# Performance work log

Hardware: AMD Instinct MI355X
Metric: run time of the kernel (lower is better)

## Reference

```python
import jax, jax.numpy as jnp
import numpy as np

EPS = 1e-5

def bn_relu(y, g, b):
    # BatchNorm1d in training mode: stats over (B, L) per channel, biased variance
    mu = jnp.mean(y, axis=(0, 2), keepdims=True)
    var = jnp.var(y, axis=(0, 2), keepdims=True)
    yn = (y - mu) * jax.lax.rsqrt(var + EPS)
    return jax.nn.relu(yn * g[None, :, None] + b[None, :, None])

def conv1x1_pad1(x, W):
    # Conv1d(k=1, padding=1, bias=False): pointwise matmul then zero-pad length by 1 each side
    y = jnp.einsum('bcl,oc->bol', x, W)
    return jnp.pad(y, ((0, 0), (0, 0), (1, 1)))

def conv1x1(x, W, b):
    return jnp.einsum('bcl,oc->bol', x, W) + b[None, :, None]

def conv3_pad1(x, W):
    # Conv1d(k=3, padding=1, bias=False); W: [O, C, 3]
    return jax.lax.conv_general_dilated(x, W, window_strides=(1,), padding=((1, 1),),
                                        dimension_numbers=('NCH', 'OIH', 'NCH'))

def pam(f, Wq, bq, Wk, bk, Wv, bv, gamma):
    q = conv1x1(f, Wq, bq)          # [B, C//8, L]
    k = conv1x1(f, Wk, bk)          # [B, C//8, L]
    v = conv1x1(f, Wv, bv)          # [B, C, L]
    energy = jnp.einsum('bql,bqm->blm', q, k)   # [B, L, L]
    attn = jax.nn.softmax(energy, axis=-1)
    out = jnp.einsum('bcm,blm->bcl', v, attn)
    return gamma * out + f

def cam(f, gamma):
    energy = jnp.einsum('bcl,bdl->bcd', f, f)    # [B, C, C]
    energy_new = jnp.max(energy, axis=-1, keepdims=True) - energy
    attn = jax.nn.softmax(energy_new, axis=-1)
    out = jnp.einsum('bcd,bdl->bcl', attn, f)
    return gamma * out + f

def setup_inputs() -> dict:
    key = jax.random.key(0)
    ks = jax.random.split(key, 24)
    B, C, L = 8, 256, 2046
    IC, OC = C // 4, 128  # inter_channels=64, out_channels
    s = 0.05
    d = {
        'x':   jax.random.normal(ks[0], (B, C, L), jnp.float32),
        'W5a': jax.random.normal(ks[1], (IC, C), jnp.float32) * s,
        'g5a': jnp.ones((IC,), jnp.float32), 'b5a': jnp.zeros((IC,), jnp.float32),
        'W5c': jax.random.normal(ks[2], (IC, C), jnp.float32) * s,
        'g5c': jnp.ones((IC,), jnp.float32), 'b5c': jnp.zeros((IC,), jnp.float32),
        'Wq':  jax.random.normal(ks[3], (IC // 8, IC), jnp.float32) * s,
        'bq':  jnp.zeros((IC // 8,), jnp.float32),
        'Wk':  jax.random.normal(ks[4], (IC // 8, IC), jnp.float32) * s,
        'bk':  jnp.zeros((IC // 8,), jnp.float32),
        'Wv':  jax.random.normal(ks[5], (IC, IC), jnp.float32) * s,
        'bv':  jnp.zeros((IC,), jnp.float32),
        'gamma_pam': jnp.full((1,), 0.1, jnp.float32),
        'gamma_cam': jnp.full((1,), 0.1, jnp.float32),
        'W51': jax.random.normal(ks[6], (IC, IC, 3), jnp.float32) * s,
        'g51': jnp.ones((IC,), jnp.float32), 'b51': jnp.zeros((IC,), jnp.float32),
        'W52': jax.random.normal(ks[7], (IC, IC, 3), jnp.float32) * s,
        'g52': jnp.ones((IC,), jnp.float32), 'b52': jnp.zeros((IC,), jnp.float32),
        'W6':  jax.random.normal(ks[8], (OC, IC), jnp.float32) * s,
        'b6':  jnp.zeros((OC,), jnp.float32),
        'W7':  jax.random.normal(ks[9], (OC, IC), jnp.float32) * s,
        'b7':  jnp.zeros((OC,), jnp.float32),
        'W8':  jax.random.normal(ks[10], (OC, IC), jnp.float32) * s,
        'b8':  jnp.zeros((OC,), jnp.float32),
    }
    return d

def reference(x, W5a, g5a, b5a, W5c, g5c, b5c, Wq, bq, Wk, bk, Wv, bv,
              gamma_pam, gamma_cam, W51, g51, b51, W52, g52, b52,
              W6, b6, W7, b7, W8, b8):
    # dropout (p=0.1) treated as identity (eval mode)
    feat1 = bn_relu(conv1x1_pad1(x, W5a), g5a, b5a)          # [B, IC, L+2]
    sa_feat = pam(feat1, Wq, bq, Wk, bk, Wv, bv, gamma_pam)
    sa_conv = bn_relu(conv3_pad1(sa_feat, W51), g51, b51)
    sa_output = conv1x1(sa_conv, W6, b6)                     # [B, OC, L+2]
    feat2 = bn_relu(conv1x1_pad1(x, W5c), g5c, b5c)
    sc_feat = cam(feat2, gamma_cam)
    sc_conv = bn_relu(conv3_pad1(sc_feat, W52), g52, b52)
    sc_output = conv1x1(sc_conv, W7, b7)
    feat_sum = sa_conv + sc_conv
    sasc = conv1x1(feat_sum, W8, b8)
    # pool == 'maxpool' selects AdaptiveAvgPool1d(1) in the original (note swap)
    sasc = jnp.mean(sasc, axis=-1)                            # [B, OC]
    return (sasc, sa_output, sc_output)
```

## Files before the change

### kernel.cpp

```cpp
#include <hip/hip_runtime.h>
#include <math.h>

#define B 8
#define C 256
#define L 2046
#define LP 2048
#define IC 64
#define OC 128
#define BN_EPS 1e-5f
#define INVN (1.f / 16384.f)

#define OFF_Y1T    0u
#define OFF_Y2C    524288u
#define OFF_SAFT   1048576u
#define OFF_SCFT   1572864u
#define OFF_Y51T   2097152u
#define OFF_Y52T   2621440u
#define OFF_VB     3145728u
#define OFF_QT     3670016u
#define OFF_KT     3735552u
#define OFF_LPART  3801088u
#define OFF_EPART  3866624u
#define OFF_ATTN   4390912u
#define OFF_STATS1 4423680u
#define OFF_STATS2 4424704u
#define OFF_W5BF   4425728u
#define OFF_W67    4442112u
#define OFF_WT     4450304u
#define OFF_WQKV   4462592u
#define OFF_BQKV   4465152u

typedef __attribute__((ext_vector_type(8))) short bshort8;
typedef __attribute__((ext_vector_type(4))) float f32x4;

__device__ __forceinline__ unsigned short f2bf(float f) {
    union { float f; unsigned int u; } v; v.f = f;
    return (unsigned short)((v.u + 0x8000u) >> 16);
}
__device__ __forceinline__ float bf2f(unsigned short u) {
    union { unsigned int i; float f; } v; v.i = ((unsigned int)u) << 16;
    return v.f;
}
__device__ __forceinline__ unsigned int pk2(float a, float b) {
    union { float f; unsigned int u; } va, vb; va.f = a; vb.f = b;
    return __builtin_amdgcn_perm(vb.u + 0x8000u, va.u + 0x8000u, 0x07060302u);
}

__device__ __forceinline__ void load_coef(const float* __restrict__ STATS,
        const float* __restrict__ g, const float* __restrict__ beta,
        int base, int cnt, float* cA, float* cB) {
    int t = threadIdx.x;
    if (t < cnt) {
        int ch = base + t;
        float s = STATS[ch * 2] + STATS[256 + ch * 2] + STATS[512 + ch * 2] + STATS[768 + ch * 2];
        float q = STATS[ch * 2 + 1] + STATS[256 + ch * 2 + 1] + STATS[512 + ch * 2 + 1] + STATS[768 + ch * 2 + 1];
        float mu = s * INVN;
        float var = q * INVN - mu * mu;
        float A = g[t] * rsqrtf(var + BN_EPS);
        cA[t] = A;
        cB[t] = beta[t] - mu * A;
    }
}

__global__ __launch_bounds__(256) void k_wprep(
        const float* __restrict__ W5a, const float* __restrict__ W5c,
        const float* __restrict__ W6, const float* __restrict__ W7,
        const float* __restrict__ W51, const float* __restrict__ W52,
        const float* __restrict__ Wq, const float* __restrict__ Wk,
        const float* __restrict__ Wv, const float* __restrict__ bq,
        const float* __restrict__ bk, const float* __restrict__ bv,
        const float* __restrict__ b8,
        unsigned short* __restrict__ W5BF, unsigned short* __restrict__ W67,
        unsigned short* __restrict__ WT, unsigned short* __restrict__ WQKV,
        float* __restrict__ BQKV, float* __restrict__ STATS1,
        float* __restrict__ STATS2, float* __restrict__ out_sasc) {
    int i = blockIdx.x * 256 + threadIdx.x;
    if (i < 32768) {
        int o = i >> 8, c = i & 255;
        W5BF[i] = f2bf(o < 64 ? W5a[o * 256 + c] : W5c[(o - 64) * 256 + c]);
    } else if (i < 49152) {
        int j = i - 32768; int g = j >> 13; int r = j & 8191;
        W67[j] = f2bf(g ? W7[r] : W6[r]);
    } else if (i < 73728) {
        int j = i - 49152;
        int c = j & 63, o = (j >> 6) & 63, wt = j >> 12; int w = wt / 3, t = wt % 3;
        const float* Ws = w ? W52 : W51;
        WT[j] = f2bf(Ws[(o * 64 + c) * 3 + t]);
    } else if (i < 78848) {
        int j = i - 73728; int o = j >> 6, c = j & 63;
        float v = o < 8 ? Wq[o * 64 + c] : (o < 16 ? Wk[(o - 8) * 64 + c] : Wv[(o - 16) * 64 + c]);
        WQKV[j] = f2bf(v);
    } else if (i < 78928) {
        int o = i - 78848;
        BQKV[o] = o < 8 ? bq[o] : (o < 16 ? bk[o - 8] : bv[o - 16]);
    } else if (i < 80976) {
        int j = i - 78928;
        if (j < 1024) STATS1[j] = 0.f; else STATS2[j - 1024] = 0.f;
    } else if (i < 82000) {
        int j = i - 80976;
        out_sasc[j] = b8[j & 127];
    }
}

__global__ __launch_bounds__(256) void k_conv1(const float* __restrict__ x,
        const unsigned short* __restrict__ W5BF,
        unsigned short* __restrict__ Y1T, unsigned short* __restrict__ Y2C,
        float* __restrict__ STATS1) {
    __shared__ unsigned short xt[64][264];
    __shared__ float lds_part[4][64];
    int lt = blockIdx.x, b = blockIdx.y;
    int l0 = lt * 64;
    int t = threadIdx.x;
    {
        int j = t & 63, cg = t >> 6;
        int ls = l0 - 1 + j;
        bool ok = (ls >= 0) && (ls < L);
        const float* xs = x + (size_t)(b * C + cg * 64) * L + ls;
        unsigned short* row = &xt[j][cg * 64];
#pragma unroll 8
        for (int cc = 0; cc < 64; ++cc) {
            float v = ok ? xs[(size_t)cc * L] : 0.f;
            row[cc] = f2bf(v);
        }
    }
    __syncthreads();
    int w = t >> 6, lane = t & 63, n = lane & 15, quad = lane >> 4;
    bshort8 wf[2][8];
#pragma unroll
    for (int oi = 0; oi < 2; ++oi)
#pragma unroll
        for (int kt = 0; kt < 8; ++kt)
            wf[oi][kt] = *(const bshort8*)(W5BF + (size_t)((w * 2 + oi) * 16 + n) * C + kt * 32 + quad * 8);
    f32x4 acc[2][4];
#pragma unroll
    for (int oi = 0; oi < 2; ++oi)
#pragma unroll
        for (int sub = 0; sub < 4; ++sub) acc[oi][sub] = (f32x4){0.f, 0.f, 0.f, 0.f};
#pragma unroll
    for (int sub = 0; sub < 4; ++sub) {
        int lloc = sub * 16 + n;
#pragma unroll
        for (int kt = 0; kt < 8; ++kt) {
            bshort8 xb = *(const bshort8*)(&xt[lloc][kt * 32 + quad * 8]);
            acc[0][sub] = __builtin_amdgcn_mfma_f32_16x16x32_bf16(wf[0][kt], xb, acc[0][sub], 0, 0, 0);
            acc[1][sub] = __builtin_amdgcn_mfma_f32_16x16x32_bf16(wf[1][kt], xb, acc[1][sub], 0, 0, 0);
        }
    }
    if (w < 2) {
#pragma unroll
        for (int sub = 0; sub < 4; ++sub) {
            int lp = l0 + sub * 16 + n;
#pragma unroll
            for (int oi = 0; oi < 2; ++oi) {
                int ot = w * 2 + oi;
                uint2 pv;
                pv.x = pk2(acc[oi][sub][0], acc[oi][sub][1]);
                pv.y = pk2(acc[oi][sub][2], acc[oi][sub][3]);
                *(uint2*)(Y1T + ((size_t)(b * LP + lp)) * IC + ot * 16 + quad * 4) = pv;
            }
        }
    } else {
#pragma unroll
        for (int oi = 0; oi < 2; ++oi) {
            int ot = (w - 2) * 2 + oi;
#pragma unroll
            for (int r = 0; r < 4; ++r) {
                int o = ot * 16 + quad * 4 + r;
                unsigned short* dst = Y2C + ((size_t)(b * IC + o)) * LP + l0;
#pragma unroll
                for (int sub = 0; sub < 4; ++sub)
                    dst[sub * 16 + n] = f2bf(acc[oi][sub][r]);
            }
        }
    }
#pragma unroll
    for (int oi = 0; oi < 2; ++oi)
#pragma unroll
        for (int r = 0; r < 4; ++r) {
            float s = 0.f, q = 0.f;
#pragma unroll
            for (int sub = 0; sub < 4; ++sub) {
                float v = acc[oi][sub][r];
                s += v; q += v * v;
            }
#pragma unroll
            for (int msk = 1; msk < 16; msk <<= 1) {
                s += __shfl_xor(s, msk, 64);
                q += __shfl_xor(q, msk, 64);
            }
            if (n == 0) {
                int ci = oi * 16 + quad * 4 + r;
                lds_part[w][ci * 2] = s;
                lds_part[w][ci * 2 + 1] = q;
            }
        }
    __syncthreads();
    {
        int ch = t >> 1, wsrc = ch >> 5;
        int idx = ((ch & 31) << 1) | (t & 1);
        atomicAdd(&STATS1[(blockIdx.x & 3) * 256 + t], lds_part[wsrc][idx]);
    }
}

__device__ void role_qkv(char* dynsm, int lt, int b,
        const unsigned short* __restrict__ Y1T, const float* __restrict__ STATS1,
        const float* __restrict__ g5a, const float* __restrict__ b5a,
        const unsigned short* __restrict__ WQKV, const float* __restrict__ BQKV,
        unsigned short* __restrict__ QT, unsigned short* __restrict__ KT,
        unsigned short* __restrict__ VB) {
    float* cA = (float*)dynsm;
    float* cB = cA + 64;
    load_coef(STATS1, g5a, b5a, 0, 64, cA, cB);
    __syncthreads();
    int t = threadIdx.x;
    int w = t >> 6, lane = t & 63, n = lane & 15, quad = lane >> 4;
    int lrow = lt * 64 + w * 16 + n;
    bshort8 fb[2];
#pragma unroll
    for (int kt = 0; kt < 2; ++kt) {
        bshort8 raw = *(const bshort8*)(Y1T + ((size_t)(b * LP + lrow)) * IC + kt * 32 + quad * 8);
        bshort8 f;
#pragma unroll
        for (int j = 0; j < 8; ++j) {
            int c = kt * 32 + quad * 8 + j;
            float v = fmaxf(fmaf(cA[c], bf2f((unsigned short)raw[j]), cB[c]), 0.f);
            ((unsigned short*)&f)[j] = f2bf(v);
        }
        fb[kt] = f;
    }
    f32x4 acc[5];
#pragma unroll
    for (int ot = 0; ot < 5; ++ot) {
        f32x4 a = {0.f, 0.f, 0.f, 0.f};
#pragma unroll
        for (int kt = 0; kt < 2; ++kt) {
            bshort8 wf = *(const bshort8*)(WQKV + (size_t)(ot * 16 + n) * IC + kt * 32 + quad * 8);
            a = __builtin_amdgcn_mfma_f32_16x16x32_bf16(wf, fb[kt], a, 0, 0, 0);
        }
        acc[ot] = a;
    }
#pragma unroll
    for (int ot = 0; ot < 5; ++ot)
#pragma unroll
        for (int r = 0; r < 4; ++r) {
            int o = ot * 16 + quad * 4 + r;
            unsigned short bv16 = f2bf(acc[ot][r] + BQKV[o]);
            if (ot == 0) {
                if (o < 8) QT[((size_t)(b * LP + lrow)) * 8 + o] = bv16;
                else KT[((size_t)(b * LP + lrow)) * 8 + (o - 8)] = bv16;
            } else {
                VB[((size_t)(b * IC + (o - 16))) * LP + lrow] = bv16;
            }
        }
}

__device__ void role_gram(char* dynsm, int blk, int b,
        const unsigned short* __restrict__ Y2C, const float* __restrict__ STATS1,
        const float* __restrict__ g5c, const float* __restrict__ b5c,
        float* __restrict__ EPART) {
    float* cA = (float*)dynsm;
    float* cB = cA + 64;
    load_coef(STATS1, g5c, b5c, 64, 64, cA, cB);
    __syncthreads();
    int t = threadIdx.x;
    int w = t >> 6, lane = t & 63, n = lane & 15, quad = lane >> 4;
    f32x4 acc[4][4];
#pragma unroll
    for (int ti = 0; ti < 4; ++ti)
#pragma unroll
        for (int tj = 0; tj < 4; ++tj) acc[ti][tj] = (f32x4){0.f, 0.f, 0.f, 0.f};
    for (int chunk = 0; chunk < 4; ++chunk) {
        int lb = (blk * 4 + w) * 128 + chunk * 32 + quad * 8;
        bshort8 frag[4];
#pragma unroll
        for (int g = 0; g < 4; ++g) {
            int c = g * 16 + n;
            bshort8 raw = *(const bshort8*)(Y2C + ((size_t)(b * IC + c)) * LP + lb);
            bshort8 f;
            float A = cA[c], Bc = cB[c];
#pragma unroll
            for (int j = 0; j < 8; ++j)
                ((unsigned short*)&f)[j] = f2bf(fmaxf(fmaf(A, bf2f((unsigned short)raw[j]), Bc), 0.f));
            frag[g] = f;
        }
#pragma unroll
        for (int ti = 0; ti < 4; ++ti)
#pragma unroll
            for (int tj = 0; tj < 4; ++tj)
                acc[ti][tj] = __builtin_amdgcn_mfma_f32_16x16x32_bf16(frag[ti], frag[tj], acc[ti][tj], 0, 0, 0);
    }
    float* ep = EPART + ((size_t)(b * 16 + blk * 4 + w)) * 4096;
#pragma unroll
    for (int ti = 0; ti < 4; ++ti)
#pragma unroll
        for (int tj = 0; tj < 4; ++tj)
#pragma unroll
            for (int r = 0; r < 4; ++r)
                ep[(ti * 16 + quad * 4 + r) * 64 + tj * 16 + n] = acc[ti][tj][r];
}

__global__ __launch_bounds__(256) void k_fuse1(
        const unsigned short* __restrict__ Y1T, const unsigned short* __restrict__ Y2C,
        const float* __restrict__ STATS1,
        const float* __restrict__ g5a, const float* __restrict__ b5a,
        const float* __restrict__ g5c, const float* __restrict__ b5c,
        const unsigned short* __restrict__ WQKV, const float* __restrict__ BQKV,
        unsigned short* __restrict__ QT, unsigned short* __restrict__ KT,
        unsigned short* __restrict__ VB, float* __restrict__ EPART) {
    extern __shared__ char dynsm[];
    int idx = blockIdx.x;
    if (idx < 256) role_qkv(dynsm, idx & 31, idx >> 5, Y1T, STATS1, g5a, b5a,
                            WQKV, BQKV, QT, KT, VB);
    else { int g = idx - 256; role_gram(dynsm, g & 3, g >> 2, Y2C, STATS1, g5c, b5c, EPART); }
}

__device__ void role_pam(char* dynsm, int qt, int ks, int b,
        const unsigned short* __restrict__ qT, const unsigned short* __restrict__ kT,
        const unsigned short* __restrict__ vb,
        unsigned short* __restrict__ OPART, float* __restrict__ LPART) {
    unsigned short* vs = (unsigned short*)dynsm;
    unsigned short* ps = vs + 4608;
    float* os = (float*)dynsm;
    int l0 = qt * 64;
    int tid = threadIdx.x;
    int wq = tid >> 6, lane = tid & 63, n = lane & 15, quad = lane >> 4;
    bshort8 qa = {};
    if (quad == 0)
        qa = *(const bshort8*)(qT + ((size_t)(b * LP + l0 + wq * 16 + n)) * 8);
    f32x4 acc[4];
#pragma unroll
    for (int s = 0; s < 4; ++s) acc[s] = (f32x4){0.f, 0.f, 0.f, 0.f};
    float li[4] = {0.f, 0.f, 0.f, 0.f};
    unsigned short* pw = ps + wq * 16 * 72;

    for (int it = 0; it < 8; ++it) {
        int m0 = ks * 512 + it * 64;
        __syncthreads();
        {
            int row = tid >> 2, chn = tid & 3;
            const unsigned short* src = vb + ((size_t)(b * IC + row)) * LP + m0 + chn * 16;
            unsigned short* dstl = vs + row * 72 + chn * 16;
            *(bshort8*)dstl = *(const bshort8*)src;
            *(bshort8*)(dstl + 8) = *(const bshort8*)(src + 8);
        }
        bshort8 kb[4];
#pragma unroll
        for (int s = 0; s < 4; ++s) kb[s] = (bshort8){};
        if (quad == 0) {
#pragma unroll
            for (int s = 0; s < 4; ++s)
                kb[s] = *(const bshort8*)(kT + ((size_t)(b * LP + m0 + s * 16 + n)) * 8);
        }
        __syncthreads();
        f32x4 sc[4];
#pragma unroll
        for (int s = 0; s < 4; ++s)
            sc[s] = __builtin_amdgcn_mfma_f32_16x16x32_bf16(qa, kb[s],
                        (f32x4){0.f, 0.f, 0.f, 0.f}, 0, 0, 0);
#pragma unroll
        for (int s = 0; s < 4; ++s)
#pragma unroll
            for (int r = 0; r < 4; ++r) {
                float p = __expf(sc[s][r]);
                li[r] += p;
                pw[(quad * 4 + r) * 72 + s * 16 + n] = f2bf(p);
            }
#pragma unroll
        for (int step = 0; step < 2; ++step) {
            bshort8 pa = *(const bshort8*)(pw + n * 72 + step * 32 + quad * 8);
#pragma unroll
            for (int s = 0; s < 4; ++s) {
                bshort8 vf = *(const bshort8*)(vs + (s * 16 + n) * 72 + step * 32 + quad * 8);
                acc[s] = __builtin_amdgcn_mfma_f32_16x16x32_bf16(pa, vf, acc[s], 0, 0, 0);
            }
        }
    }
    __syncthreads();
#pragma unroll
    for (int s = 0; s < 4; ++s)
#pragma unroll
        for (int r = 0; r < 4; ++r)
            os[(s * 16 + n) * 65 + wq * 16 + quad * 4 + r] = acc[s][r];
    size_t lbase = ((size_t)((b * 32 + qt) * 4 + ks)) * 64;
#pragma unroll
    for (int r = 0; r < 4; ++r) {
        float s_ = li[r];
#pragma unroll
        for (int msk = 1; msk < 16; msk <<= 1) s_ += __shfl_xor(s_, msk, 64);
        if (n == 0) LPART[lbase + wq * 16 + quad * 4 + r] = s_;
    }
    __syncthreads();
    size_t ob = ((size_t)((b * 32 + qt) * 4 + ks)) * 4096;
    int c = tid >> 2, qc = tid & 3;
    unsigned int* od = (unsigned int*)(OPART + ob + c * 64 + qc * 16);
#pragma unroll
    for (int i = 0; i < 8; ++i)
        od[i] = pk2(os[c * 65 + qc * 16 + 2 * i], os[c * 65 + qc * 16 + 2 * i + 1]);
}

__device__ void role_cam_softmax(char* dynsm, int b,
        const float* __restrict__ EPART, float* __restrict__ attn) {
    float* e = (float*)dynsm;
    int t = threadIdx.x;
    for (int idx = t; idx < 4096; idx += 256) {
        float s = 0.f;
        for (int ch = 0; ch < 16; ++ch) s += EPART[((size_t)(b * 16 + ch)) * 4096 + idx];
        e[idx] = s;
    }
    __syncthreads();
    if (t < 64) {
        float mn = INFINITY;
        for (int d = 0; d < 64; ++d) mn = fminf(mn, e[t * 64 + d]);
        float s = 0.f;
        float* a = attn + (size_t)b * 4096 + t * 64;
        for (int d = 0; d < 64; ++d) { float p = __expf(mn - e[t * 64 + d]); a[d] = p; s += p; }
        float inv = 1.f / s;
        for (int d = 0; d < 64; ++d) a[d] *= inv;
    }
}

__global__ __launch_bounds__(256) void k_fuse2(
        const unsigned short* __restrict__ QT, const unsigned short* __restrict__ KT,
        const unsigned short* __restrict__ VB,
        unsigned short* __restrict__ OPART, float* __restrict__ LPART,
        const float* __restrict__ EPART, float* __restrict__ ATTN) {
    extern __shared__ char dynsm[];
    int idx = blockIdx.x;
    if (idx < 1024) role_pam(dynsm, idx & 31, (idx >> 5) & 3, idx >> 7, QT, KT, VB, OPART, LPART);
    else role_cam_softmax(dynsm, idx - 1024, EPART, ATTN);
}

__device__ void role_pam_combine(char* dynsm, int qt, int b,
        const unsigned short* __restrict__ OPART, const float* __restrict__ LPART,
        const unsigned short* __restrict__ Y1T, const float* __restrict__ STATS1,
        const float* __restrict__ g5a, const float* __restrict__ b5a,
        const float* __restrict__ gamma, unsigned short* __restrict__ SAFT) {
    float* dn = (float*)dynsm;
    float* cA = dn + 64;
    float* cB = cA + 64;
    unsigned short* tile = (unsigned short*)(cB + 64);
    int l0 = qt * 64;
    int t = threadIdx.x;
    load_coef(STATS1, g5a, b5a, 0, 64, cA, cB);
    if (t < 64) {
        size_t lbase = ((size_t)((b * 32 + qt) * 4)) * 64;
        dn[t] = LPART[lbase + t] + LPART[lbase + 64 + t] +
                LPART[lbase + 128 + t] + LPART[lbase + 192 + t];
    }
    __syncthreads();
    int c = t >> 2, qc = t & 3;
    float O[16];
#pragma unroll
    for (int i = 0; i < 16; ++i) O[i] = 0.f;
    size_t ob = ((size_t)((b * 32 + qt) * 4)) * 4096 + c * 64 + qc * 16;
#pragma unroll
    for (int s = 0; s < 4; ++s) {
        bshort8 p0 = *(const bshort8*)(OPART + ob + (size_t)s * 4096);
        bshort8 p1 = *(const bshort8*)(OPART + ob + (size_t)s * 4096 + 8);
#pragma unroll
        for (int i = 0; i < 8; ++i) {
            O[i]     += bf2f((unsigned short)p0[i]);
            O[8 + i] += bf2f((unsigned short)p1[i]);
        }
    }
    float gm = gamma[0];
#pragma unroll
    for (int i = 0; i < 16; ++i) {
        int q = qc * 16 + i;
        unsigned short raw = Y1T[((size_t)(b * LP + l0 + q)) * IC + c];
        float f1v = fmaxf(fmaf(cA[c], bf2f(raw), cB[c]), 0.f);
        float val = fmaf(gm, O[i] / dn[q], f1v);
        tile[q * 66 + c] = f2bf(val);
    }
    __syncthreads();
    int li = t >> 2, cc = t & 3;
    unsigned int* dst = (unsigned int*)(SAFT + ((size_t)(b * LP + l0 + li)) * IC + cc * 16);
#pragma unroll
    for (int i = 0; i < 8; ++i)
        dst[i] = *(unsigned int*)(tile + li * 66 + cc * 16 + 2 * i);
}

__device__ void role_cam_apply(char* dynsm, int blkx, int b,
        const float* __restrict__ attn, const unsigned short* __restrict__ Y2C,
        const float* __restrict__ STATS1,
        const float* __restrict__ g5c, const float* __restrict__ b5c,
        const float* __restrict__ gamma, unsigned short* __restrict__ SCFT) {
    float* as = (float*)dynsm;
    float* cA = as + 4096;
    float* cB = cA + 64;
    unsigned short* tile = (unsigned short*)(cB + 64);
    int l0 = blkx * 128;
    int t = threadIdx.x;
    int lq = t & 127, ch = t >> 7;
    load_coef(STATS1, g5c, b5c, 64, 64, cA, cB);
    for (int i = t; i < 4096; i += 256) as[i] = attn[(size_t)b * 4096 + i];
    __syncthreads();
    float acc[32];
#pragma unroll
    for (int i = 0; i < 32; ++i) acc[i] = 0.f;
    const unsigned short* fb = Y2C + (size_t)b * IC * LP + l0 + lq;
    for (int d4 = 0; d4 < 16; ++d4) {
        float fv[4];
#pragma unroll
        for (int i = 0; i < 4; ++i) {
            int d = 4 * d4 + i;
            fv[i] = fmaxf(fmaf(cA[d], bf2f(fb[(size_t)d * LP]), cB[d]), 0.f);
        }
#pragma unroll
        for (int cc = 0; cc < 32; ++cc) {
            const float4 a4 = *reinterpret_cast<const float4*>(as + (ch * 32 + cc) * 64 + d4 * 4);
            acc[cc] += a4.x * fv[0] + a4.y * fv[1] + a4.z * fv[2] + a4.w * fv[3];
        }
    }
    float gm = gamma[0];
#pragma unroll
    for (int cc = 0; cc < 32; ++cc) {
        int c = ch * 32 + cc;
        float res = fmaxf(fmaf(cA[c], bf2f(fb[(size_t)c * LP]), cB[c]), 0.f);
        tile[lq * 66 + c] = f2bf(fmaf(gm, acc[cc], res));
    }
    __syncthreads();
    int li = t >> 1, half = t & 1;
    unsigned int* dst = (unsigned int*)(SCFT + ((size_t)(b * LP + l0 + li)) * IC + half * 32);
#pragma unroll
    for (int i = 0; i < 16; ++i)
        dst[i] = *(unsigned int*)(tile + li * 66 + half * 32 + 2 * i);
}

__global__ __launch_bounds__(256) void k_fuse3(
        const unsigned short* __restrict__ OPART, const float* __restrict__ LPART,
        const unsigned short* __restrict__ Y1T, const unsigned short* __restrict__ Y2C,
        const float* __restrict__ STATS1,
        const float* __restrict__ g5a, const float* __restrict__ b5a,
        const float* __restrict__ g5c, const float* __restrict__ b5c,
        const float* __restrict__ gpam, const float* __restrict__ gcam,
        const float* __restrict__ ATTN,
        unsigned short* __restrict__ SAFT, unsigned short* __restrict__ SCFT) {
    extern __shared__ char dynsm[];
    int idx = blockIdx.x;
    if (idx < 256) role_pam_combine(dynsm, idx & 31, idx >> 5, OPART, LPART, Y1T,
                                    STATS1, g5a, b5a, gpam, SAFT);
    else { int g = idx - 256; role_cam_apply(dynsm, g & 15, g >> 4, ATTN, Y2C,
                                             STATS1, g5c, b5c, gcam, SCFT); }
}

__global__ __launch_bounds__(256) void k_conv3(const unsigned short* __restrict__ SAFT,
        const unsigned short* __restrict__ SCFT, const unsigned short* __restrict__ WTall,
        unsigned short* __restrict__ Y51T, unsigned short* __restrict__ Y52T,
        float* __restrict__ STATS2) {
    __shared__ float lds_part[4][128];
    int lt = blockIdx.x, og = blockIdx.y, b = blockIdx.z;
    const unsigned short* FTsrc = og ? SCFT : SAFT;
    const unsigned short* WT = WTall + og * 12288;
    unsigned short* dst = og ? Y52T : Y51T;
    int l0 = lt * 64;
    int w = threadIdx.x >> 6, lane = threadIdx.x & 63, n = lane & 15, quad = lane >> 4;
    int lrow = l0 + w * 16 + n;
    f32x4 acc[4];
#pragma unroll
    for (int ot = 0; ot < 4; ++ot) acc[ot] = (f32x4){0.f, 0.f, 0.f, 0.f};
#pragma unroll
    for (int t3 = 0; t3 < 3; ++t3) {
        int row = lrow + t3 - 1;
        bshort8 fb[2];
#pragma unroll
        for (int kt = 0; kt < 2; ++kt) {
            if (row >= 0 && row < LP)
                fb[kt] = *(const bshort8*)(FTsrc + ((size_t)(b * LP + row)) * IC + kt * 32 + quad * 8);
            else fb[kt] = (bshort8){};
        }
#pragma unroll
        for (int ot = 0; ot < 4; ++ot)
#pragma unroll
            for (int kt = 0; kt < 2; ++kt) {
                bshort8 wf = *(const bshort8*)(WT + ((size_t)(t3 * 64 + ot * 16 + n)) * IC + kt * 32 + quad * 8);
                acc[ot] = __builtin_amdgcn_mfma_f32_16x16x32_bf16(wf, fb[kt], acc[ot], 0, 0, 0);
            }
    }
#pragma unroll
    for (int ot = 0; ot < 4; ++ot) {
        uint2 pv;
        pv.x = pk2(acc[ot][0], acc[ot][1]);
        pv.y = pk2(acc[ot][2], acc[ot][3]);
        *(uint2*)(dst + ((size_t)(b * LP + lrow)) * IC + ot * 16 + quad * 4) = pv;
    }
#pragma unroll
    for (int ot = 0; ot < 4; ++ot)
#pragma unroll
        for (int r = 0; r < 4; ++r) {
            float s = acc[ot][r], q = s * s;
#pragma unroll
            for (int msk = 1; msk < 16; msk <<= 1) {
                s += __shfl_xor(s, msk, 64);
                q += __shfl_xor(q, msk, 64);
            }
            if (n == 0) {
                int cch = ot * 16 + quad * 4 + r;
                lds_part[w][cch * 2] = s;
                lds_part[w][cch * 2 + 1] = q;
            }
        }
    __syncthreads();
    int t = threadIdx.x;
    if (t < 128) {
        float s = lds_part[0][t] + lds_part[1][t] + lds_part[2][t] + lds_part[3][t];
        atomicAdd(&STATS2[(blockIdx.x & 3) * 256 + og * 128 + t], s);
    }
}

__global__ __launch_bounds__(256) void k_final(const unsigned short* __restrict__ Y51T,
        const unsigned short* __restrict__ Y52T, const float* __restrict__ STATS2,
        const float* __restrict__ g51, const float* __restrict__ b51,
        const float* __restrict__ g52, const float* __restrict__ b52,
        const unsigned short* __restrict__ W67,
        const float* __restrict__ b6, const float* __restrict__ b7,
        const float* __restrict__ W8,
        float* __restrict__ out_sa, float* __restrict__ out_sc,
        float* __restrict__ out_sasc) {
    __shared__ float cA[128], cB[128];
    __shared__ float fsw[4][64];
    __shared__ float chsum[64];
    int lt = blockIdx.x, og = blockIdx.y, b = blockIdx.z;
    int t = threadIdx.x;
    if (t < 128) {
        float s = STATS2[t * 2] + STATS2[256 + t * 2] + STATS2[512 + t * 2] + STATS2[768 + t * 2];
        float q = STATS2[t * 2 + 1] + STATS2[256 + t * 2 + 1] + STATS2[512 + t * 2 + 1] + STATS2[768 + t * 2 + 1];
        float mu = s * INVN, var = q * INVN - mu * mu;
        float gv = t < 64 ? g51[t] : g52[t - 64];
        float bv = t < 64 ? b51[t] : b52[t - 64];
        float A = gv * rsqrtf(var + BN_EPS);
        cA[t] = A; cB[t] = bv - mu * A;
    }
    __syncthreads();
    int w = t >> 6, lane = t & 63, n = lane & 15, quad = lane >> 4;
    int lrow = lt * 64 + w * 16 + n;
    float fs_lane[16];
    bshort8 ba[2], bb[2];
#pragma unroll
    for (int kt = 0; kt < 2; ++kt) {
        bshort8 ra = *(const bshort8*)(Y51T + ((size_t)(b * LP + lrow)) * IC + kt * 32 + quad * 8);
        bshort8 rb = *(const bshort8*)(Y52T + ((size_t)(b * LP + lrow)) * IC + kt * 32 + quad * 8);
        bshort8 fa, fb;
#pragma unroll
        for (int j = 0; j < 8; ++j) {
            int c = kt * 32 + quad * 8 + j;
            float v1 = fmaxf(fmaf(cA[c], bf2f((unsigned short)ra[j]), cB[c]), 0.f);
            float v2 = fmaxf(fmaf(cA[64 + c], bf2f((unsigned short)rb[j]), cB[64 + c]), 0.f);
            ((unsigned short*)&fa)[j] = f2bf(v1);
            ((unsigned short*)&fb)[j] = f2bf(v2);
            fs_lane[kt * 8 + j] = v1 + v2;
        }
        ba[kt] = fa; bb[kt] = fb;
    }
    f32x4 accA[4], accB[4];
#pragma unroll
    for (int ot = 0; ot < 4; ++ot) {
        accA[ot] = (f32x4){0.f, 0.f, 0.f, 0.f};
        accB[ot] = (f32x4){0.f, 0.f, 0.f, 0.f};
    }
#pragma unroll
    for (int ot = 0; ot < 4; ++ot)
#pragma unroll
        for (int kt = 0; kt < 2; ++kt) {
            bshort8 wa = *(const bshort8*)(W67 + (size_t)(og * 64 + ot * 16 + n) * IC + kt * 32 + quad * 8);
            bshort8 wb = *(const bshort8*)(W67 + 8192 + (size_t)(og * 64 + ot * 16 + n) * IC + kt * 32 + quad * 8);
            accA[ot] = __builtin_amdgcn_mfma_f32_16x16x32_bf16(wa, ba[kt], accA[ot], 0, 0, 0);
            accB[ot] = __builtin_amdgcn_mfma_f32_16x16x32_bf16(wb, bb[kt], accB[ot], 0, 0, 0);
        }
#pragma unroll
    for (int ot = 0; ot < 4; ++ot)
#pragma unroll
        for (int r = 0; r < 4; ++r) {
            int o = og * 64 + ot * 16 + quad * 4 + r;
            out_sa[((size_t)(b * OC + o)) * LP + lrow] = accA[ot][r] + b6[o];
            out_sc[((size_t)(b * OC + o)) * LP + lrow] = accB[ot][r] + b7[o];
        }
    if (og == 0) {
#pragma unroll
        for (int i = 0; i < 16; ++i) {
            float s = fs_lane[i];
#pragma unroll
            for (int msk = 1; msk < 16; msk <<= 1) s += __shfl_xor(s, msk, 64);
            if (n == 0) {
                int c = (i >> 3) * 32 + quad * 8 + (i & 7);
                fsw[w][c] = s;
            }
        }
        __syncthreads();
        if (t < 64) chsum[t] = fsw[0][t] + fsw[1][t] + fsw[2][t] + fsw[3][t];
        __syncthreads();
        if (t < 128) {
            float s = 0.f;
            for (int c = 0; c < 64; ++c) s = fmaf(W8[t * 64 + c], chsum[c], s);
            atomicAdd(&out_sasc[b * OC + t], s * (1.f / (float)LP));
        }
    }
}

extern "C" void kernel_launch(void* const* d_in, const int* in_sizes, int n_in,
                              void* d_out, int out_size, void* d_ws, size_t ws_size,
                              hipStream_t stream) {
    (void)in_sizes; (void)n_in; (void)out_size; (void)ws_size;
    const float* x    = (const float*)d_in[0];
    const float* W5a  = (const float*)d_in[1];
    const float* g5a  = (const float*)d_in[2];
    const float* b5a  = (const float*)d_in[3];
    const float* W5c  = (const float*)d_in[4];
    const float* g5c  = (const float*)d_in[5];
    const float* b5c  = (const float*)d_in[6];
    const float* Wq   = (const float*)d_in[7];
    const float* bq   = (const float*)d_in[8];
    const float* Wk   = (const float*)d_in[9];
    const float* bk   = (const float*)d_in[10];
    const float* Wv   = (const float*)d_in[11];
    const float* bv   = (const float*)d_in[12];
    const float* gpam = (const float*)d_in[13];
    const float* gcam = (const float*)d_in[14];
    const float* W51  = (const float*)d_in[15];
    const float* g51  = (const float*)d_in[16];
    const float* b51  = (const float*)d_in[17];
    const float* W52  = (const float*)d_in[18];
    const float* g52  = (const float*)d_in[19];
    const float* b52  = (const float*)d_in[20];
    const float* W6   = (const float*)d_in[21];
    const float* b6   = (const float*)d_in[22];
    const float* W7   = (const float*)d_in[23];
    const float* b7   = (const float*)d_in[24];
    const float* W8   = (const float*)d_in[25];
    const float* b8   = (const float*)d_in[26];

    float* ws = (float*)d_ws;
    float* out = (float*)d_out;
    unsigned short* Y1T  = (unsigned short*)(ws + OFF_Y1T);
    unsigned short* Y2C  = (unsigned short*)(ws + OFF_Y2C);
    unsigned short* SAFT = (unsigned short*)(ws + OFF_SAFT);
    unsigned short* SCFT = (unsigned short*)(ws + OFF_SCFT);
    unsigned short* Y51T = (unsigned short*)(ws + OFF_Y51T);
    unsigned short* Y52T = (unsigned short*)(ws + OFF_Y52T);
    unsigned short* VB   = (unsigned short*)(ws + OFF_VB);
    unsigned short* QT   = (unsigned short*)(ws + OFF_QT);
    unsigned short* KT   = (unsigned short*)(ws + OFF_KT);
    float* LPART  = ws + OFF_LPART;
    float* EPART  = ws + OFF_EPART;
    float* ATTN   = ws + OFF_ATTN;
    float* STATS1 = ws + OFF_STATS1;
    float* STATS2 = ws + OFF_STATS2;
    unsigned short* W5BF = (unsigned short*)(ws + OFF_W5BF);
    unsigned short* W67  = (unsigned short*)(ws + OFF_W67);
    unsigned short* WT   = (unsigned short*)(ws + OFF_WT);
    unsigned short* WQKV = (unsigned short*)(ws + OFF_WQKV);
    float* BQKV = ws + OFF_BQKV;

    float* out_sa = out + B * OC;
    float* out_sc = out + B * OC + (size_t)B * OC * LP;
    unsigned short* OPART = (unsigned short*)out_sa;

    k_wprep<<<321, 256, 0, stream>>>(W5a, W5c, W6, W7, W51, W52, Wq, Wk, Wv,
                                     bq, bk, bv, b8, W5BF, W67, WT, WQKV, BQKV,
                                     STATS1, STATS2, out);
    k_conv1<<<dim3(32, B), 256, 0, stream>>>(x, W5BF, Y1T, Y2C, STATS1);
    k_fuse1<<<288, 256, 512, stream>>>(Y1T, Y2C, STATS1, g5a, b5a, g5c, b5c,
                                       WQKV, BQKV, QT, KT, VB, EPART);
    k_fuse2<<<1032, 256, 18432, stream>>>(QT, KT, VB, OPART, LPART, EPART, ATTN);
    k_fuse3<<<384, 256, 33792, stream>>>(OPART, LPART, Y1T, Y2C, STATS1,
                                         g5a, b5a, g5c, b5c, gpam, gcam, ATTN,
                                         SAFT, SCFT);
    k_conv3<<<dim3(32, 2, B), 256, 0, stream>>>(SAFT, SCFT, WT, Y51T, Y52T, STATS2);
    k_final<<<dim3(32, 2, B), 256, 0, stream>>>(Y51T, Y52T, STATS2, g51, b51, g52, b52,
                                                W67, b6, b7, W8, out_sa, out_sc, out);
}
```

Baseline: 235.5 us.

## Fuse PAM/CAM apply with conv3 via halo tiles; double-buffer V in PAM

The PAM-combine and CAM-apply roles now build a 66-row LDS tile that includes halo rows recomputed from neighbour data, then run the k=3 conv with MFMA straight from that tile. This removes the SAFT/SCFT intermediates and the separate k_conv3 launch. The CAM role moves to 64-wide L tiles, giving 512 blocks. Separately, the PAM attention loop double-buffers V tiles in LDS with one barrier per iteration instead of two, at the cost of more shared memory per block and redundant halo recomputation (a serial 64-term dot product per halo element in CAM).

```diff
diff --git a/kernel.cpp b/kernel.cpp
--- a/kernel.cpp
+++ b/kernel.cpp
@@ -12,8 +12,6 @@
 
 #define OFF_Y1T    0u
 #define OFF_Y2C    524288u
-#define OFF_SAFT   1048576u
-#define OFF_SCFT   1572864u
 #define OFF_Y51T   2097152u
 #define OFF_Y52T   2621440u
 #define OFF_VB     3145728u
@@ -318,12 +316,14 @@
         const unsigned short* __restrict__ qT, const unsigned short* __restrict__ kT,
         const unsigned short* __restrict__ vb,
         unsigned short* __restrict__ OPART, float* __restrict__ LPART) {
-    unsigned short* vs = (unsigned short*)dynsm;
-    unsigned short* ps = vs + 4608;
+    unsigned short* vs0 = (unsigned short*)dynsm;
+    unsigned short* vs1 = vs0 + 4608;
+    unsigned short* ps  = vs1 + 4608;
     float* os = (float*)dynsm;
     int l0 = qt * 64;
     int tid = threadIdx.x;
     int wq = tid >> 6, lane = tid & 63, n = lane & 15, quad = lane >> 4;
+    int srow = tid >> 2, schn = tid & 3;
     bshort8 qa = {};
     if (quad == 0)
         qa = *(const bshort8*)(qT + ((size_t)(b * LP + l0 + wq * 16 + n)) * 8);
@@ -333,16 +333,23 @@
     float li[4] = {0.f, 0.f, 0.f, 0.f};
     unsigned short* pw = ps + wq * 16 * 72;
 
+    {
+        const unsigned short* src = vb + ((size_t)(b * IC + srow)) * LP + ks * 512 + schn * 16;
+        unsigned short* d = vs0 + srow * 72 + schn * 16;
+        *(bshort8*)d = *(const bshort8*)src;
+        *(bshort8*)(d + 8) = *(const bshort8*)(src + 8);
+    }
+    __syncthreads();
     for (int it = 0; it < 8; ++it) {
+        unsigned short* cur = (it & 1) ? vs1 : vs0;
+        unsigned short* nxt = (it & 1) ? vs0 : vs1;
+        if (it < 7) {
+            const unsigned short* src = vb + ((size_t)(b * IC + srow)) * LP + ks * 512 + (it + 1) * 64 + schn * 16;
+            unsigned short* d = nxt + srow * 72 + schn * 16;
+            *(bshort8*)d = *(const bshort8*)src;
+            *(bshort8*)(d + 8) = *(const bshort8*)(src + 8);
+        }
         int m0 = ks * 512 + it * 64;
-        __syncthreads();
-        {
-            int row = tid >> 2, chn = tid & 3;
-            const unsigned short* src = vb + ((size_t)(b * IC + row)) * LP + m0 + chn * 16;
-            unsigned short* dstl = vs + row * 72 + chn * 16;
-            *(bshort8*)dstl = *(const bshort8*)src;
-            *(bshort8*)(dstl + 8) = *(const bshort8*)(src + 8);
-        }
         bshort8 kb[4];
 #pragma unroll
         for (int s = 0; s < 4; ++s) kb[s] = (bshort8){};
@@ -351,7 +358,6 @@
             for (int s = 0; s < 4; ++s)
                 kb[s] = *(const bshort8*)(kT + ((size_t)(b * LP + m0 + s * 16 + n)) * 8);
         }
-        __syncthreads();
         f32x4 sc[4];
 #pragma unroll
         for (int s = 0; s < 4; ++s)
@@ -370,12 +376,12 @@
             bshort8 pa = *(const bshort8*)(pw + n * 72 + step * 32 + quad * 8);
 #pragma unroll
             for (int s = 0; s < 4; ++s) {
-                bshort8 vf = *(const bshort8*)(vs + (s * 16 + n) * 72 + step * 32 + quad * 8);
+                bshort8 vf = *(const bshort8*)(cur + (s * 16 + n) * 72 + step * 32 + quad * 8);
                 acc[s] = __builtin_amdgcn_mfma_f32_16x16x32_bf16(pa, vf, acc[s], 0, 0, 0);
             }
         }
-    }
-    __syncthreads();
+        __syncthreads();
+    }
 #pragma unroll
     for (int s = 0; s < 4; ++s)
 #pragma unroll
@@ -430,15 +436,69 @@
     else role_cam_softmax(dynsm, idx - 1024, EPART, ATTN);
 }
 
-__device__ void role_pam_combine(char* dynsm, int qt, int b,
+__device__ __forceinline__ void conv3_from_tile(const unsigned short* tile,
+        const unsigned short* __restrict__ WT, unsigned short* __restrict__ dst,
+        int b, int l0, float* lds_part, float* __restrict__ STATS2,
+        int og, int blockx) {
+    int t = threadIdx.x;
+    int w = t >> 6, lane = t & 63, n = lane & 15, quad = lane >> 4;
+    int lrow = l0 + w * 16 + n;
+    f32x4 acc[4];
+#pragma unroll
+    for (int ot = 0; ot < 4; ++ot) acc[ot] = (f32x4){0.f, 0.f, 0.f, 0.f};
+#pragma unroll
+    for (int t3 = 0; t3 < 3; ++t3) {
+        int trow = w * 16 + n + t3;
+        bshort8 fb0 = *(const bshort8*)(tile + trow * 72 + quad * 8);
+        bshort8 fb1 = *(const bshort8*)(tile + trow * 72 + 32 + quad * 8);
+#pragma unroll
+        for (int ot = 0; ot < 4; ++ot) {
+            bshort8 w0 = *(const bshort8*)(WT + ((size_t)(t3 * 64 + ot * 16 + n)) * IC + quad * 8);
+            bshort8 w1 = *(const bshort8*)(WT + ((size_t)(t3 * 64 + ot * 16 + n)) * IC + 32 + quad * 8);
+            acc[ot] = __builtin_amdgcn_mfma_f32_16x16x32_bf16(w0, fb0, acc[ot], 0, 0, 0);
+            acc[ot] = __builtin_amdgcn_mfma_f32_16x16x32_bf16(w1, fb1, acc[ot], 0, 0, 0);
+        }
+    }
+#pragma unroll
+    for (int ot = 0; ot < 4; ++ot) {
+        uint2 pv;
+        pv.x = pk2(acc[ot][0], acc[ot][1]);
+        pv.y = pk2(acc[ot][2], acc[ot][3]);
+        *(uint2*)(dst + ((size_t)(b * LP + lrow)) * IC + ot * 16 + quad * 4) = pv;
+    }
+#pragma unroll
+    for (int ot = 0; ot < 4; ++ot)
+#pragma unroll
+        for (int r = 0; r < 4; ++r) {
+            float s = acc[ot][r], q = s * s;
+#pragma unroll
+            for (int msk = 1; msk < 16; msk <<= 1) {
+                s += __shfl_xor(s, msk, 64);
+                q += __shfl_xor(q, msk, 64);
+            }
+            if (n == 0) {
+                int cch = ot * 16 + quad * 4 + r;
+                lds_part[w * 128 + cch * 2] = s;
+                lds_part[w * 128 + cch * 2 + 1] = q;
+            }
+        }
+    __syncthreads();
+    if (t < 128) {
+        float s = lds_part[t] + lds_part[128 + t] + lds_part[256 + t] + lds_part[384 + t];
+        atomicAdd(&STATS2[(blockx & 3) * 256 + og * 128 + t], s);
+    }
+}
+
+__device__ void role_pam_c3(char* dynsm, int qt, int b,
         const unsigned short* __restrict__ OPART, const float* __restrict__ LPART,
         const unsigned short* __restrict__ Y1T, const float* __restrict__ STATS1,
         const float* __restrict__ g5a, const float* __restrict__ b5a,
-        const float* __restrict__ gamma, unsigned short* __restrict__ SAFT) {
+        const float* __restrict__ gamma, const unsigned short* __restrict__ WT,
+        unsigned short* __restrict__ Y51T, float* __restrict__ STATS2) {
     float* dn = (float*)dynsm;
-    float* cA = dn + 64;
-    float* cB = cA + 64;
+    float* cA = dn + 64; float* cB = cA + 64;
     unsigned short* tile = (unsigned short*)(cB + 64);
+    float* lds_part = (float*)(tile + 4752);
     int l0 = qt * 64;
     int t = threadIdx.x;
     load_coef(STATS1, g5a, b5a, 0, 64, cA, cB);
@@ -448,164 +508,133 @@
                 LPART[lbase + 128 + t] + LPART[lbase + 192 + t];
     }
     __syncthreads();
-    int c = t >> 2, qc = t & 3;
-    float O[16];
-#pragma unroll
-    for (int i = 0; i < 16; ++i) O[i] = 0.f;
-    size_t ob = ((size_t)((b * 32 + qt) * 4)) * 4096 + c * 64 + qc * 16;
-#pragma unroll
-    for (int s = 0; s < 4; ++s) {
-        bshort8 p0 = *(const bshort8*)(OPART + ob + (size_t)s * 4096);
-        bshort8 p1 = *(const bshort8*)(OPART + ob + (size_t)s * 4096 + 8);
-#pragma unroll
-        for (int i = 0; i < 8; ++i) {
-            O[i]     += bf2f((unsigned short)p0[i]);
-            O[8 + i] += bf2f((unsigned short)p1[i]);
-        }
-    }
     float gm = gamma[0];
-#pragma unroll
-    for (int i = 0; i < 16; ++i) {
-        int q = qc * 16 + i;
-        unsigned short raw = Y1T[((size_t)(b * LP + l0 + q)) * IC + c];
-        float f1v = fmaxf(fmaf(cA[c], bf2f(raw), cB[c]), 0.f);
-        float val = fmaf(gm, O[i] / dn[q], f1v);
-        tile[q * 66 + c] = f2bf(val);
-    }
-    __syncthreads();
-    int li = t >> 2, cc = t & 3;
-    unsigned int* dst = (unsigned int*)(SAFT + ((size_t)(b * LP + l0 + li)) * IC + cc * 16);
-#pragma unroll
-    for (int i = 0; i < 8; ++i)
-        dst[i] = *(unsigned int*)(tile + li * 66 + cc * 16 + 2 * i);
-}
-
-__device__ void role_cam_apply(char* dynsm, int blkx, int b,
+    {
+        int c = t >> 2, qc = t & 3;
+        float O[16];
+#pragma unroll
+        for (int i = 0; i < 16; ++i) O[i] = 0.f;
+        size_t ob = ((size_t)((b * 32 + qt) * 4)) * 4096 + c * 64 + qc * 16;
+#pragma unroll
+        for (int s = 0; s < 4; ++s) {
+            bshort8 p0 = *(const bshort8*)(OPART + ob + (size_t)s * 4096);
+            bshort8 p1 = *(const bshort8*)(OPART + ob + (size_t)s * 4096 + 8);
+#pragma unroll
+            for (int i = 0; i < 8; ++i) {
+                O[i]     += bf2f((unsigned short)p0[i]);
+                O[8 + i] += bf2f((unsigned short)p1[i]);
+            }
+        }
+#pragma unroll
+        for (int i = 0; i < 16; ++i) {
+            int q = qc * 16 + i;
+            unsigned short raw = Y1T[((size_t)(b * LP + l0 + q)) * IC + c];
+            float f1v = fmaxf(fmaf(cA[c], bf2f(raw), cB[c]), 0.f);
+            tile[(1 + q) * 72 + c] = f2bf(fmaf(gm, O[i] / dn[q], f1v));
+        }
+    }
+    if (t < 128) {
+        int row = (t & 1) ? 65 : 0;
+        int ch = t >> 1;
+        int l = l0 - 1 + row;
+        float val = 0.f;
+        if (l >= 0 && l < LP) {
+            int qh = l >> 6, lih = l & 63;
+            size_t lb2 = ((size_t)((b * 32 + qh) * 4)) * 64;
+            float dnh = LPART[lb2 + lih] + LPART[lb2 + 64 + lih] +
+                        LPART[lb2 + 128 + lih] + LPART[lb2 + 192 + lih];
+            size_t ob2 = ((size_t)((b * 32 + qh) * 4)) * 4096 + ch * 64 + lih;
+            float Oh = bf2f(OPART[ob2]) + bf2f(OPART[ob2 + 4096]) +
+                       bf2f(OPART[ob2 + 8192]) + bf2f(OPART[ob2 + 12288]);
+            float f1v = fmaxf(fmaf(cA[ch], bf2f(Y1T[((size_t)(b * LP + l)) * IC + ch]), cB[ch]), 0.f);
+            val = fmaf(gm, Oh / dnh, f1v);
+        }
+        tile[row * 72 + ch] = f2bf(val);
+    }
+    __syncthreads();
+    conv3_from_tile(tile, WT, Y51T, b, l0, lds_part, STATS2, 0, qt);
+}
+
+__device__ void role_cam_c3(char* dynsm, int lt, int b,
         const float* __restrict__ attn, const unsigned short* __restrict__ Y2C,
         const float* __restrict__ STATS1,
         const float* __restrict__ g5c, const float* __restrict__ b5c,
-        const float* __restrict__ gamma, unsigned short* __restrict__ SCFT) {
+        const float* __restrict__ gamma, const unsigned short* __restrict__ WT,
+        unsigned short* __restrict__ Y52T, float* __restrict__ STATS2) {
     float* as = (float*)dynsm;
-    float* cA = as + 4096;
-    float* cB = cA + 64;
+    float* cA = as + 4096; float* cB = cA + 64;
     unsigned short* tile = (unsigned short*)(cB + 64);
-    int l0 = blkx * 128;
-    int t = threadIdx.x;
-    int lq = t & 127, ch = t >> 7;
+    float* lds_part = (float*)(tile + 4752);
+    int l0 = lt * 64;
+    int t = threadIdx.x;
     load_coef(STATS1, g5c, b5c, 64, 64, cA, cB);
     for (int i = t; i < 4096; i += 256) as[i] = attn[(size_t)b * 4096 + i];
     __syncthreads();
-    float acc[32];
-#pragma unroll
-    for (int i = 0; i < 32; ++i) acc[i] = 0.f;
-    const unsigned short* fb = Y2C + (size_t)b * IC * LP + l0 + lq;
-    for (int d4 = 0; d4 < 16; ++d4) {
-        float fv[4];
-#pragma unroll
-        for (int i = 0; i < 4; ++i) {
-            int d = 4 * d4 + i;
-            fv[i] = fmaxf(fmaf(cA[d], bf2f(fb[(size_t)d * LP]), cB[d]), 0.f);
-        }
-#pragma unroll
-        for (int cc = 0; cc < 32; ++cc) {
-            const float4 a4 = *reinterpret_cast<const float4*>(as + (ch * 32 + cc) * 64 + d4 * 4);
-            acc[cc] += a4.x * fv[0] + a4.y * fv[1] + a4.z * fv[2] + a4.w * fv[3];
-        }
-    }
     float gm = gamma[0];
-#pragma unroll
-    for (int cc = 0; cc < 32; ++cc) {
-        int c = ch * 32 + cc;
-        float res = fmaxf(fmaf(cA[c], bf2f(fb[(size_t)c * LP]), cB[c]), 0.f);
-        tile[lq * 66 + c] = f2bf(fmaf(gm, acc[cc], res));
-    }
-    __syncthreads();
-    int li = t >> 1, half = t & 1;
-    unsigned int* dst = (unsigned int*)(SCFT + ((size_t)(b * LP + l0 + li)) * IC + half * 32);
-#pragma unroll
-    for (int i = 0; i < 16; ++i)
-        dst[i] = *(unsigned int*)(tile + li * 66 + half * 32 + 2 * i);
-}
-
-__global__ __launch_bounds__(256) void k_fuse3(
+    {
+        int lq = t & 63, cg = t >> 6;
+        const unsigned short* fb = Y2C + (size_t)b * IC * LP + l0 + lq;
+        float acc[16];
+#pragma unroll
+        for (int i = 0; i < 16; ++i) acc[i] = 0.f;
+        for (int d4 = 0; d4 < 16; ++d4) {
+            float fv[4];
+#pragma unroll
+            for (int i = 0; i < 4; ++i) {
+                int d = 4 * d4 + i;
+                fv[i] = fmaxf(fmaf(cA[d], bf2f(fb[(size_t)d * LP]), cB[d]), 0.f);
+            }
+#pragma unroll
+            for (int cc = 0; cc < 16; ++cc) {
+                const float4 a4 = *reinterpret_cast<const float4*>(as + (cg * 16 + cc) * 64 + d4 * 4);
+                acc[cc] += a4.x * fv[0] + a4.y * fv[1] + a4.z * fv[2] + a4.w * fv[3];
+            }
+        }
+#pragma unroll
+        for (int cc = 0; cc < 16; ++cc) {
+            int c = cg * 16 + cc;
+            float res = fmaxf(fmaf(cA[c], bf2f(fb[(size_t)c * LP]), cB[c]), 0.f);
+            tile[(1 + lq) * 72 + c] = f2bf(fmaf(gm, acc[cc], res));
+        }
+    }
+    if (t < 128) {
+        int row = (t & 1) ? 65 : 0;
+        int ch = t >> 1;
+        int l = l0 - 1 + row;
+        float val = 0.f;
+        if (l >= 0 && l < LP) {
+            const unsigned short* fb = Y2C + (size_t)b * IC * LP + l;
+            float a = 0.f;
+            for (int d = 0; d < 64; ++d) {
+                float fv = fmaxf(fmaf(cA[d], bf2f(fb[(size_t)d * LP]), cB[d]), 0.f);
+                a = fmaf(as[ch * 64 + d], fv, a);
+            }
+            float res = fmaxf(fmaf(cA[ch], bf2f(fb[(size_t)ch * LP]), cB[ch]), 0.f);
+            val = fmaf(gm, a, res);
+        }
+        tile[row * 72 + ch] = f2bf(val);
+    }
+    __syncthreads();
+    conv3_from_tile(tile, WT, Y52T, b, l0, lds_part, STATS2, 1, lt);
+}
+
+__global__ __launch_bounds__(256) void k_fuse3c(
         const unsigned short* __restrict__ OPART, const float* __restrict__ LPART,
         const unsigned short* __restrict__ Y1T, const unsigned short* __restrict__ Y2C,
         const float* __restrict__ STATS1,
         const float* __restrict__ g5a, const float* __restrict__ b5a,
         const float* __restrict__ g5c, const float* __restrict__ b5c,
         const float* __restrict__ gpam, const float* __restrict__ gcam,
-        const float* __restrict__ ATTN,
-        unsigned short* __restrict__ SAFT, unsigned short* __restrict__ SCFT) {
+        const float* __restrict__ ATTN, const unsigned short* __restrict__ WTall,
+        unsigned short* __restrict__ Y51T, unsigned short* __restrict__ Y52T,
+        float* __restrict__ STATS2) {
     extern __shared__ char dynsm[];
     int idx = blockIdx.x;
-    if (idx < 256) role_pam_combine(dynsm, idx & 31, idx >> 5, OPART, LPART, Y1T,
-                                    STATS1, g5a, b5a, gpam, SAFT);
-    else { int g = idx - 256; role_cam_apply(dynsm, g & 15, g >> 4, ATTN, Y2C,
-                                             STATS1, g5c, b5c, gcam, SCFT); }
-}
-
-__global__ __launch_bounds__(256) void k_conv3(const unsigned short* __restrict__ SAFT,
-        const unsigned short* __restrict__ SCFT, const unsigned short* __restrict__ WTall,
-        unsigned short* __restrict__ Y51T, unsigned short* __restrict__ Y52T,
-        float* __restrict__ STATS2) {
-    __shared__ float lds_part[4][128];
-    int lt = blockIdx.x, og = blockIdx.y, b = blockIdx.z;
-    const unsigned short* FTsrc = og ? SCFT : SAFT;
-    const unsigned short* WT = WTall + og * 12288;
-    unsigned short* dst = og ? Y52T : Y51T;
-    int l0 = lt * 64;
-    int w = threadIdx.x >> 6, lane = threadIdx.x & 63, n = lane & 15, quad = lane >> 4;
-    int lrow = l0 + w * 16 + n;
-    f32x4 acc[4];
-#pragma unroll
-    for (int ot = 0; ot < 4; ++ot) acc[ot] = (f32x4){0.f, 0.f, 0.f, 0.f};
-#pragma unroll
-    for (int t3 = 0; t3 < 3; ++t3) {
-        int row = lrow + t3 - 1;
-        bshort8 fb[2];
-#pragma unroll
-        for (int kt = 0; kt < 2; ++kt) {
-            if (row >= 0 && row < LP)
-                fb[kt] = *(const bshort8*)(FTsrc + ((size_t)(b * LP + row)) * IC + kt * 32 + quad * 8);
-            else fb[kt] = (bshort8){};
-        }
-#pragma unroll
-        for (int ot = 0; ot < 4; ++ot)
-#pragma unroll
-            for (int kt = 0; kt < 2; ++kt) {
-                bshort8 wf = *(const bshort8*)(WT + ((size_t)(t3 * 64 + ot * 16 + n)) * IC + kt * 32 + quad * 8);
-                acc[ot] = __builtin_amdgcn_mfma_f32_16x16x32_bf16(wf, fb[kt], acc[ot], 0, 0, 0);
-            }
-    }
-#pragma unroll
-    for (int ot = 0; ot < 4; ++ot) {
-        uint2 pv;
-        pv.x = pk2(acc[ot][0], acc[ot][1]);
-        pv.y = pk2(acc[ot][2], acc[ot][3]);
-        *(uint2*)(dst + ((size_t)(b * LP + lrow)) * IC + ot * 16 + quad * 4) = pv;
-    }
-#pragma unroll
-    for (int ot = 0; ot < 4; ++ot)
-#pragma unroll
-        for (int r = 0; r < 4; ++r) {
-            float s = acc[ot][r], q = s * s;
-#pragma unroll
-            for (int msk = 1; msk < 16; msk <<= 1) {
-                s += __shfl_xor(s, msk, 64);
-                q += __shfl_xor(q, msk, 64);
-            }
-            if (n == 0) {
-                int cch = ot * 16 + quad * 4 + r;
-                lds_part[w][cch * 2] = s;
-                lds_part[w][cch * 2 + 1] = q;
-            }
-        }
-    __syncthreads();
-    int t = threadIdx.x;
-    if (t < 128) {
-        float s = lds_part[0][t] + lds_part[1][t] + lds_part[2][t] + lds_part[3][t];
-        atomicAdd(&STATS2[(blockIdx.x & 3) * 256 + og * 128 + t], s);
-    }
+    if (idx < 256) role_pam_c3(dynsm, idx & 31, idx >> 5, OPART, LPART, Y1T,
+                               STATS1, g5a, b5a, gpam, WTall, Y51T, STATS2);
+    else { int g = idx - 256; role_cam_c3(dynsm, g & 31, g >> 5, ATTN, Y2C,
+                                          STATS1, g5c, b5c, gcam, WTall + 12288,
+                                          Y52T, STATS2); }
 }
 
 __global__ __launch_bounds__(256) void k_final(const unsigned short* __restrict__ Y51T,
@@ -733,8 +762,6 @@
     float* out = (float*)d_out;
     unsigned short* Y1T  = (unsigned short*)(ws + OFF_Y1T);
     unsigned short* Y2C  = (unsigned short*)(ws + OFF_Y2C);
-    unsigned short* SAFT = (unsigned short*)(ws + OFF_SAFT);
-    unsigned short* SCFT = (unsigned short*)(ws + OFF_SCFT);
     unsigned short* Y51T = (unsigned short*)(ws + OFF_Y51T);
     unsigned short* Y52T = (unsigned short*)(ws + OFF_Y52T);
     unsigned short* VB   = (unsigned short*)(ws + OFF_VB);
@@ -761,11 +788,10 @@
     k_conv1<<<dim3(32, B), 256, 0, stream>>>(x, W5BF, Y1T, Y2C, STATS1);
     k_fuse1<<<288, 256, 512, stream>>>(Y1T, Y2C, STATS1, g5a, b5a, g5c, b5c,
                                        WQKV, BQKV, QT, KT, VB, EPART);
-    k_fuse2<<<1032, 256, 18432, stream>>>(QT, KT, VB, OPART, LPART, EPART, ATTN);
-    k_fuse3<<<384, 256, 33792, stream>>>(OPART, LPART, Y1T, Y2C, STATS1,
-                                         g5a, b5a, g5c, b5c, gpam, gcam, ATTN,
-                                         SAFT, SCFT);
-    k_conv3<<<dim3(32, 2, B), 256, 0, stream>>>(SAFT, SCFT, WT, Y51T, Y52T, STATS2);
+    k_fuse2<<<1032, 256, 27648, stream>>>(QT, KT, VB, OPART, LPART, EPART, ATTN);
+    k_fuse3c<<<512, 256, 28448, stream>>>(OPART, LPART, Y1T, Y2C, STATS1,
+                                          g5a, b5a, g5c, b5c, gpam, gcam, ATTN,
+                                          WT, Y51T, Y52T, STATS2);
     k_final<<<dim3(32, 2, B), 256, 0, stream>>>(Y51T, Y52T, STATS2, g51, b51, g52, b52,
                                                 W67, b6, b7, W8, out_sa, out_sc, out);
 }
```

After: 214.9 us. -8.8%, faster.
